# Optimization experiments

Measured on AMD Instinct MI355X. Metric: run time of the kernel, lower is better.

Reference implementation:

```python
import jax, jax.numpy as jnp
import numpy as np
import math

D_MODEL = 1024
N_HEADS = 16
D_K = D_MODEL // N_HEADS
THRESH = 0.1  # attention probs below this are zeroed


def setup_inputs() -> dict:
    key = jax.random.key(0)
    ks = jax.random.split(key, 9)
    B, S, D = 2, 2048, D_MODEL
    scale = 1.0 / math.sqrt(D)
    x = jax.random.normal(ks[0], (B, S, D), dtype=jnp.float32)
    Wq = jax.random.normal(ks[1], (D, D), dtype=jnp.float32) * scale
    bq = jax.random.normal(ks[2], (D,), dtype=jnp.float32) * 0.01
    Wk = jax.random.normal(ks[3], (D, D), dtype=jnp.float32) * scale
    bk = jax.random.normal(ks[4], (D,), dtype=jnp.float32) * 0.01
    Wv = jax.random.normal(ks[5], (D, D), dtype=jnp.float32) * scale
    bv = jax.random.normal(ks[6], (D,), dtype=jnp.float32) * 0.01
    Wo = jax.random.normal(ks[7], (D, D), dtype=jnp.float32) * scale
    bo = jax.random.normal(ks[8], (D,), dtype=jnp.float32) * 0.01
    return {"x": x, "Wq": Wq, "bq": bq, "Wk": Wk, "bk": bk,
            "Wv": Wv, "bv": bv, "Wo": Wo, "bo": bo}


def _split_heads(t):
    B, S, D = t.shape
    return t.reshape(B, S, N_HEADS, D_K).transpose(0, 2, 1, 3)  # [B,H,S,dk]


def reference(x, Wq, bq, Wk, bk, Wv, bv, Wo, bo):
    # torch nn.Linear: y = x @ W.T + b
    q = _split_heads(x @ Wq.T + bq)
    k = _split_heads(x @ Wk.T + bk)
    v = _split_heads(x @ Wv.T + bv)
    scores = jnp.einsum('bhqd,bhkd->bhqk', q, k) / math.sqrt(D_K)
    probs = jax.nn.softmax(scores, axis=-1)          # full unmasked softmax (returned)
    keep = probs >= THRESH                            # ~low_attention_mask
    probs_model = jnp.where(keep, probs, 0.0)        # masked_fill; dropout is identity in eval
    ctx = jnp.einsum('bhqk,bhkd->bhqd', probs_model, v)
    B, H, S, dk = ctx.shape
    merged = ctx.transpose(0, 2, 1, 3).reshape(B, S, H * dk)
    out = merged @ Wo.T + bo
    attention_sum = probs.sum(axis=1)                # [B,S,S] sum over heads
    attention_mask = keep.astype(jnp.float32).sum(axis=1)  # [B,S,S]
    return (out, attention_sum, attention_mask)
```

## Files before the change

### kernel.cpp

```cpp
#include <hip/hip_runtime.h>

#define SDIM 2048
#define DDIM 1024
#define NH 16
#define DK 64
#define NB 2
#define MROWS (NB * SDIM)
#define MAXEV 65536
#define EXPC 0.18033688011112f
#define L01 -3.3219281f

typedef _Float16 f16x8 __attribute__((ext_vector_type(8)));
typedef _Float16 f16x4 __attribute__((ext_vector_type(4)));
typedef float f32x4 __attribute__((ext_vector_type(4)));

__device__ __forceinline__ void ld_lds16(const _Float16* g, _Float16* l) {
  __builtin_amdgcn_global_load_lds(
      (const __attribute__((address_space(1))) void*)g,
      (__attribute__((address_space(3))) void*)l, 16, 0, 0);
}

__global__ __launch_bounds__(256) void cvt_f16(
    const float* __restrict__ x, const float* __restrict__ wq,
    const float* __restrict__ wk, const float* __restrict__ wv,
    _Float16* __restrict__ xh, _Float16* __restrict__ wqh,
    _Float16* __restrict__ wkh, _Float16* __restrict__ wvh) {
  int i = blockIdx.x * 256 + threadIdx.x;
  const float* src;
  _Float16* dst;
  int off;
  if (i < 1048576) {
    src = x; dst = xh; off = i;
  } else if (i < 1310720) {
    src = wq; dst = wqh; off = i - 1048576;
  } else if (i < 1572864) {
    src = wk; dst = wkh; off = i - 1310720;
  } else {
    src = wv; dst = wvh; off = i - 1572864;
  }
  float4 v = ((const float4*)src)[off];
  f16x4 h;
  h[0] = (_Float16)v.x; h[1] = (_Float16)v.y;
  h[2] = (_Float16)v.z; h[3] = (_Float16)v.w;
  ((f16x4*)dst)[off] = h;
}

__global__ __launch_bounds__(256, 2) void proj_gemm(
    const _Float16* __restrict__ xh, const _Float16* __restrict__ Wqh,
    const _Float16* __restrict__ Wkh, const _Float16* __restrict__ Wvh,
    const float* __restrict__ bq, const float* __restrict__ bk,
    const float* __restrict__ bv, _Float16* __restrict__ Qo,
    _Float16* __restrict__ Ko, float* __restrict__ Vo) {
  __shared__ _Float16 sA[128 * 64];
  __shared__ _Float16 sB[128 * 64];
  const int t = threadIdx.x;
  const int lane = t & 63, wv = t >> 6;
  const int lr = lane & 15, quad = lane >> 4;
  const int wm = wv >> 1, wn = wv & 1;
  const int m0 = blockIdx.y * 128, n0 = blockIdx.x * 128;
  const int z = blockIdx.z;
  const _Float16* Bp = z == 0 ? Wqh : (z == 1 ? Wkh : Wvh);
  const float* bias = z == 0 ? bq : (z == 1 ? bk : bv);

  const int strow = t >> 3;
  const int stchunk = t & 7;
  const int stsrc = (stchunk ^ (strow & 7)) * 8;

  f32x4 acc[4][4];
#pragma unroll
  for (int i = 0; i < 4; ++i)
#pragma unroll
    for (int j = 0; j < 4; ++j) acc[i][j] = (f32x4){0.f, 0.f, 0.f, 0.f};

  for (int k0 = 0; k0 < DDIM; k0 += 64) {
    __syncthreads();
#pragma unroll
    for (int i = 0; i < 4; ++i) {
      const int row = i * 32 + strow;
      ld_lds16(&xh[(size_t)(m0 + row) * DDIM + k0 + stsrc],
               &sA[row * 64 + stchunk * 8]);
      ld_lds16(&Bp[(size_t)(n0 + row) * DDIM + k0 + stsrc],
               &sB[row * 64 + stchunk * 8]);
    }
    __syncthreads();
    f16x8 af[4][2], bf[4][2];
#pragma unroll
    for (int i = 0; i < 4; ++i)
#pragma unroll
      for (int kk = 0; kk < 2; ++kk) {
        const int ph = ((kk * 4 + quad) ^ (lr & 7)) * 8;
        af[i][kk] = *(const f16x8*)&sA[(wm * 64 + i * 16 + lr) * 64 + ph];
        bf[i][kk] = *(const f16x8*)&sB[(wn * 64 + i * 16 + lr) * 64 + ph];
      }
#pragma unroll
    for (int kk = 0; kk < 2; ++kk)
#pragma unroll
      for (int i = 0; i < 4; ++i)
#pragma unroll
        for (int j = 0; j < 4; ++j)
          acc[i][j] = __builtin_amdgcn_mfma_f32_16x16x32_f16(
              af[i][kk], bf[j][kk], acc[i][j], 0, 0, 0);
  }
#pragma unroll
  for (int j = 0; j < 4; ++j) {
    const int ng = n0 + wn * 64 + j * 16 + lr;
    const float bvv = bias[ng];
    const int h = ng >> 6, d = ng & 63;
#pragma unroll
    for (int i = 0; i < 4; ++i) {
#pragma unroll
      for (int r = 0; r < 4; ++r) {
        const int mg = m0 + wm * 64 + i * 16 + quad * 4 + r;
        const int b = mg >> 11, s = mg & 2047;
        const float o = acc[i][j][r] + bvv;
        const size_t off = ((size_t)(b * NH + h) * SDIM + s) * DK + d;
        if (z == 0)
          Qo[off] = (_Float16)(o * EXPC);
        else if (z == 1)
          Ko[off] = (_Float16)o;
        else
          Vo[off] = o;
      }
    }
  }
}

__global__ __launch_bounds__(256, 6) void attn_denom(
    const _Float16* __restrict__ Q, const _Float16* __restrict__ K,
    float* __restrict__ laOut) {
  __shared__ __align__(16) _Float16 KS[3 * 4096];
  const int t = threadIdx.x;
  const int lane = t & 63, wave = t >> 6;
  const int quad = lane >> 4, lr = lane & 15;
  const int id = blockIdx.x;
  const int xcd = id & 7, inner = id >> 3;
  const int bh = xcd * 4 + (inner >> 5);
  const int q0 = (inner & 31) * 64;
  const _Float16* Qh = Q + (size_t)bh * SDIM * DK;
  const _Float16* Kh = K + (size_t)bh * SDIM * DK;
  const size_t qoff = (size_t)(q0 + wave * 16 + lr) * DK + quad * 8;
  const f16x8 aq0 = *(const f16x8*)&Qh[qoff];
  const f16x8 aq1 = *(const f16x8*)&Qh[qoff + 32];
  const int strow = t >> 3, stchunk = t & 7;
  const int stsrc = (stchunk ^ (strow & 7)) * 8;
  const int ph0 = (quad ^ (lr & 7)) * 8;
  const int ph1 = ((4 + quad) ^ (lr & 7)) * 8;

#define STAGE_DN(KT, BUF)                                                  \
  {                                                                        \
    _Pragma("unroll") for (int i = 0; i < 2; ++i)                          \
        ld_lds16(&Kh[(size_t)((KT)*64 + i * 32 + strow) * DK + stsrc],     \
                 &(BUF)[(i * 32 + strow) * 64 + stchunk * 8]);             \
  }

#define COMPUTE_DN(BUF)                                                   \
  _Pragma("unroll") for (int c = 0; c < 4; ++c) {                         \
    f16x8 b0 = *(const f16x8*)&(BUF)[(c * 16 + lr) * 64 + ph0];           \
    f16x8 b1 = *(const f16x8*)&(BUF)[(c * 16 + lr) * 64 + ph1];           \
    f32x4 acc = {0.f, 0.f, 0.f, 0.f};                                     \
    acc = __builtin_amdgcn_mfma_f32_16x16x32_f16(aq0, b0, acc, 0, 0, 0);  \
    acc = __builtin_amdgcn_mfma_f32_16x16x32_f16(aq1, b1, acc, 0, 0, 0);  \
    _Pragma("unroll") for (int r = 0; r < 4; ++r)                         \
        dsum[r] += __builtin_amdgcn_exp2f(acc[r]);                        \
  }

  float dsum[4] = {0.f, 0.f, 0.f, 0.f};
  STAGE_DN(0, KS);
  int cb = 0;
#pragma unroll 1
  for (int kt = 0; kt < 32; ++kt) {
    const int nb_ = cb == 2 ? 0 : cb + 1;
    if (kt + 1 < 32) STAGE_DN(kt + 1, KS + nb_ * 4096);
    asm volatile("" ::: "memory");
    if (kt + 1 < 32)
      asm volatile("s_waitcnt vmcnt(2)" ::: "memory");
    else
      asm volatile("s_waitcnt vmcnt(0)" ::: "memory");
    __builtin_amdgcn_s_barrier();
    asm volatile("" ::: "memory");
    COMPUTE_DN(KS + cb * 4096);
    cb = nb_;
  }
#pragma unroll
  for (int m = 1; m < 16; m <<= 1)
#pragma unroll
    for (int r = 0; r < 4; ++r)
      dsum[r] += __shfl_xor(dsum[r], m, 64);
  if (lr == 0) {
#pragma unroll
    for (int r = 0; r < 4; ++r)
      laOut[(size_t)bh * SDIM + q0 + wave * 16 + quad * 4 + r] =
          -__builtin_amdgcn_logf(dsum[r]);
  }
#undef STAGE_DN
#undef COMPUTE_DN
}

__global__ __launch_bounds__(256, 6) void attn_pass2(
    const _Float16* __restrict__ Q, const _Float16* __restrict__ K,
    const float* __restrict__ la, float* __restrict__ attSum,
    float* __restrict__ attMask, float4* __restrict__ ev,
    int* __restrict__ ecnt) {
  __shared__ __align__(16) _Float16 KS[3 * 4096];
  float* Tbuf = (float*)KS;
  const int t = threadIdx.x;
  const int lane = t & 63, wave = t >> 6;
  const int quad = lane >> 4, lr = lane & 15;
  const int id = blockIdx.x;
  const int xcd = id & 7, inner = id >> 3;
  const int b = xcd >> 2;
  const int q0 = (((xcd >> 1) & 1) * 16 + (inner >> 4)) * 64;
  const int k0 = ((xcd & 1) * 16 + (inner & 15)) * 64;
  const int strow = t >> 3, stchunk = t & 7;
  const int stsrc = (stchunk ^ (strow & 7)) * 8;
  const int ph0 = (quad ^ (lr & 7)) * 8;
  const int ph1 = ((4 + quad) ^ (lr & 7)) * 8;

  const size_t qbase = ((size_t)(b * NH) * SDIM + q0 + wave * 16 + lr) * DK;
  const size_t dbase = (size_t)(b * NH) * SDIM + q0 + wave * 16 + quad * 4;
  const size_t hstep = (size_t)SDIM * DK;

  float asum[4][4] = {};
  float mxr[4] = {-1e30f, -1e30f, -1e30f, -1e30f};

  f16x8 a0c, a1c, a0n, a1n;
  float4 lavc, lavn;

#define STAGE_H(H, BUF)                                                      \
  {                                                                          \
    const _Float16* Kp =                                                     \
        K + (size_t)(b * NH + (H)) * hstep + (size_t)k0 * DK;                \
    _Pragma("unroll") for (int i = 0; i < 2; ++i)                            \
        ld_lds16(&Kp[(size_t)(i * 32 + strow) * DK + stsrc],                 \
                 &(BUF)[(i * 32 + strow) * 64 + stchunk * 8]);               \
  }

#define LOADQ_H(H, A0, A1, LV)                                               \
  {                                                                          \
    const size_t ho = (size_t)(H)*hstep;                                     \
    A0 = *(const f16x8*)&Q[qbase + ho + quad * 8];                           \
    A1 = *(const f16x8*)&Q[qbase + ho + 32 + quad * 8];                      \
    LV = *(const float4*)&la[dbase + (size_t)(H)*SDIM];                      \
  }

#define COMPUTE_H(BUF, A0, A1, LV)                                           \
  {                                                                          \
    const float lar[4] = {LV.x, LV.y, LV.z, LV.w};                           \
    _Pragma("unroll") for (int c = 0; c < 4; ++c) {                          \
      f16x8 b0 = *(const f16x8*)&(BUF)[(c * 16 + lr) * 64 + ph0];            \
      f16x8 b1 = *(const f16x8*)&(BUF)[(c * 16 + lr) * 64 + ph1];            \
      f32x4 acc = {0.f, 0.f, 0.f, 0.f};                                      \
      acc = __builtin_amdgcn_mfma_f32_16x16x32_f16(A0, b0, acc, 0, 0, 0);    \
      acc = __builtin_amdgcn_mfma_f32_16x16x32_f16(A1, b1, acc, 0, 0, 0);    \
      _Pragma("unroll") for (int r = 0; r < 4; ++r) {                        \
        const float arg = acc[r] + lar[r];                                   \
        mxr[r] = fmaxf(mxr[r], arg);                                         \
        asum[c][r] += __builtin_amdgcn_exp2f(arg);                           \
      }                                                                      \
    }                                                                        \
  }

  STAGE_H(0, KS);
  LOADQ_H(0, a0c, a1c, lavc);
  int cb = 0;
#pragma unroll 1
  for (int h = 0; h < NH; ++h) {
    const int nb_ = cb == 2 ? 0 : cb + 1;
    if (h + 1 < NH) {
      STAGE_H(h + 1, KS + nb_ * 4096);
      LOADQ_H(h + 1, a0n, a1n, lavn);
    }
    asm volatile("" ::: "memory");
    if (h + 1 < NH)
      asm volatile("s_waitcnt vmcnt(5)" ::: "memory");
    else
      asm volatile("s_waitcnt vmcnt(0)" ::: "memory");
    __builtin_amdgcn_s_barrier();
    asm volatile("" ::: "memory");
    COMPUTE_H(KS + cb * 4096, a0c, a1c, lavc);
    if (h + 1 < NH) {
      a0c = a0n; a1c = a1n; lavc = lavn;
    }
    cb = nb_;
  }
#undef STAGE_H
#undef LOADQ_H
#undef COMPUTE_H

  const float mx =
      fmaxf(fmaxf(mxr[0], mxr[1]), fmaxf(mxr[2], mxr[3]));
  if (__any(mx >= L01)) {
    float amask[4][4] = {};
#pragma unroll 1
    for (int h = 0; h < NH; ++h) {
      const _Float16* Kp =
          K + (size_t)(b * NH + h) * hstep + (size_t)k0 * DK;
      const size_t ho = (size_t)h * hstep;
      const f16x8 aq0 = *(const f16x8*)&Q[qbase + ho + quad * 8];
      const f16x8 aq1 = *(const f16x8*)&Q[qbase + ho + 32 + quad * 8];
      const float4 l4 = *(const float4*)&la[dbase + (size_t)h * SDIM];
      const float lar[4] = {l4.x, l4.y, l4.z, l4.w};
#pragma unroll 1
      for (int c = 0; c < 4; ++c) {
        const f16x8 b0 = *(const f16x8*)&Kp[(c * 16 + lr) * DK + quad * 8];
        const f16x8 b1 = *(const f16x8*)&Kp[(c * 16 + lr) * DK + 32 + quad * 8];
        f32x4 acc = {0.f, 0.f, 0.f, 0.f};
        acc = __builtin_amdgcn_mfma_f32_16x16x32_f16(aq0, b0, acc, 0, 0, 0);
        acc = __builtin_amdgcn_mfma_f32_16x16x32_f16(aq1, b1, acc, 0, 0, 0);
#pragma unroll 1
        for (int r = 0; r < 4; ++r) {
          const float p = __builtin_amdgcn_exp2f(acc[r] + lar[r]);
          if (p >= 0.1f) {
            amask[c][r] += 1.0f;
            int idx = atomicAdd(ecnt, 1);
            if (idx < MAXEV)
              ev[idx] = make_float4(
                  __int_as_float(b * NH + h),
                  __int_as_float(q0 + wave * 16 + quad * 4 + r),
                  __int_as_float(k0 + c * 16 + lr), p);
          }
        }
      }
    }
#pragma unroll
    for (int c = 0; c < 4; ++c)
#pragma unroll
      for (int r = 0; r < 4; ++r)
        if (amask[c][r] != 0.0f) {
          const size_t row = (size_t)(b * SDIM) + q0 + wave * 16 + quad * 4 + r;
          attMask[row * SDIM + k0 + c * 16 + lr] = amask[c][r];
        }
  }
  const int g8 = t >> 3;
  const int l8 = (t & 7) * 4;
  __syncthreads();
#pragma unroll
  for (int c = 0; c < 4; ++c)
#pragma unroll
    for (int r = 0; r < 4; ++r)
      Tbuf[(wave * 16 + quad * 4 + r) * 68 + c * 16 + lr] = asum[c][r];
  __syncthreads();
#pragma unroll
  for (int p = 0; p < 2; ++p)
#pragma unroll
    for (int qh = 0; qh < 2; ++qh) {
      const int row = p * 32 + g8, col = qh * 32 + l8;
      f32x4 v = *(const f32x4*)&Tbuf[row * 68 + col];
      __builtin_nontemporal_store(
          v, (f32x4*)&attSum[((size_t)(b * SDIM) + q0 + row) * SDIM + k0 + col]);
    }
}

__global__ __launch_bounds__(64) void apply_events(
    const float4* __restrict__ ev, const int* __restrict__ ecnt,
    const float* __restrict__ V, float* __restrict__ merged,
    int* __restrict__ flags) {
  int n = *ecnt;
  if (n > MAXEV) n = MAXEV;
  const int d = threadIdx.x;
  for (int e = blockIdx.x; e < n; e += gridDim.x) {
    float4 r = ev[e];
    int bh = __float_as_int(r.x);
    int q = __float_as_int(r.y);
    int kc = __float_as_int(r.z);
    float p = r.w;
    int b = bh >> 4, h = bh & 15;
    atomicAdd(&merged[((size_t)(b * SDIM + q)) * DDIM + h * DK + d],
              p * V[((size_t)bh * SDIM + kc) * DK + d]);
    if (d == 0) flags[b * SDIM + q] = 1;
  }
}

__global__ __launch_bounds__(256) void out_gemm(const float* __restrict__ A,
                                                const float* __restrict__ W,
                                                const float* __restrict__ bias,
                                                float* __restrict__ out,
                                                const int* __restrict__ flags) {
  __shared__ float As[16][68];
  __shared__ float Ws[16][68];
  __shared__ int anyF;
  const int t = threadIdx.x;
  const int tx = t & 15, ty = t >> 4;
  const int m0 = blockIdx.y * 64;
  const int n0 = blockIdx.x * 64;
  if (t == 0) anyF = 0;
  __syncthreads();
  if (t < 64 && flags[m0 + t]) anyF = 1;
  __syncthreads();
  const int nb = n0 + tx * 4;
  const float4 bv = *(const float4*)&bias[nb];
  if (!anyF) {
#pragma unroll
    for (int r = 0; r < 4; ++r)
      *(float4*)&out[(size_t)(m0 + ty * 4 + r) * DDIM + nb] = bv;
    return;
  }
  const int lr = t >> 2;
  const int lc = (t & 3) * 4;
  float acc[4][4] = {};
  for (int k0 = 0; k0 < DDIM; k0 += 16) {
    __syncthreads();
    float4 av = *(const float4*)&A[(size_t)(m0 + lr) * DDIM + k0 + lc];
    float4 wv = *(const float4*)&W[(size_t)(n0 + lr) * DDIM + k0 + lc];
    As[lc + 0][lr] = av.x; As[lc + 1][lr] = av.y;
    As[lc + 2][lr] = av.z; As[lc + 3][lr] = av.w;
    Ws[lc + 0][lr] = wv.x; Ws[lc + 1][lr] = wv.y;
    Ws[lc + 2][lr] = wv.z; Ws[lc + 3][lr] = wv.w;
    __syncthreads();
#pragma unroll
    for (int kk = 0; kk < 16; ++kk) {
      float4 a4 = *(const float4*)&As[kk][ty * 4];
      float4 b4 = *(const float4*)&Ws[kk][tx * 4];
      const float a[4] = {a4.x, a4.y, a4.z, a4.w};
      const float b[4] = {b4.x, b4.y, b4.z, b4.w};
#pragma unroll
      for (int r = 0; r < 4; ++r)
#pragma unroll
        for (int c = 0; c < 4; ++c)
          acc[r][c] = fmaf(a[r], b[c], acc[r][c]);
    }
  }
#pragma unroll
  for (int r = 0; r < 4; ++r) {
    float4 o;
    o.x = acc[r][0] + bv.x;
    o.y = acc[r][1] + bv.y;
    o.z = acc[r][2] + bv.z;
    o.w = acc[r][3] + bv.w;
    *(float4*)&out[(size_t)(m0 + ty * 4 + r) * DDIM + nb] = o;
  }
}

extern "C" void kernel_launch(void* const* d_in, const int* in_sizes, int n_in,
                              void* d_out, int out_size, void* d_ws,
                              size_t ws_size, hipStream_t stream) {
  const float* x = (const float*)d_in[0];
  const float* Wq = (const float*)d_in[1];
  const float* bq = (const float*)d_in[2];
  const float* Wk = (const float*)d_in[3];
  const float* bk = (const float*)d_in[4];
  const float* Wv = (const float*)d_in[5];
  const float* bv = (const float*)d_in[6];
  const float* Wo = (const float*)d_in[7];
  const float* bo = (const float*)d_in[8];

  float* out = (float*)d_out;
  float* attSum = out + (size_t)MROWS * DDIM;
  float* attMask = attSum + (size_t)NB * SDIM * SDIM;

  char* ws = (char*)d_ws;
  const size_t bigF = (size_t)MROWS * DDIM * sizeof(float);
  const size_t bigH = (size_t)MROWS * DDIM * sizeof(_Float16);
  const size_t wH = (size_t)DDIM * DDIM * sizeof(_Float16);
  _Float16* Qh = (_Float16*)ws;  ws += bigH;
  _Float16* Kh = (_Float16*)ws;  ws += bigH;
  float* V = (float*)ws;         ws += bigF;
  float* merged = (float*)ws;    ws += bigF;
  _Float16* xh = (_Float16*)ws;  ws += bigH;
  _Float16* Wqh = (_Float16*)ws; ws += wH;
  _Float16* Wkh = (_Float16*)ws; ws += wH;
  _Float16* Wvh = (_Float16*)ws; ws += wH;
  float* laBuf = (float*)ws;     ws += (size_t)NB * NH * SDIM * sizeof(float);
  float4* ev = (float4*)ws;      ws += (size_t)MAXEV * sizeof(float4);
  int* flags = (int*)ws;         ws += (size_t)MROWS * sizeof(int);
  int* ecnt = (int*)ws;          ws += 16;

  hipMemsetAsync(merged, 0, bigF, stream);
  hipMemsetAsync(flags, 0, (size_t)MROWS * sizeof(int), stream);
  hipMemsetAsync(ecnt, 0, 16, stream);
  hipMemsetAsync(attMask, 0, (size_t)NB * SDIM * SDIM * sizeof(float), stream);

  dim3 blk(256);
  cvt_f16<<<dim3(7168), blk, 0, stream>>>(x, Wq, Wk, Wv, xh, Wqh, Wkh, Wvh);
  proj_gemm<<<dim3(8, 32, 3), blk, 0, stream>>>(xh, Wqh, Wkh, Wvh, bq, bk, bv,
                                                Qh, Kh, V);
  attn_denom<<<dim3(1024), blk, 0, stream>>>(Qh, Kh, laBuf);
  attn_pass2<<<dim3(2048), blk, 0, stream>>>(Qh, Kh, laBuf, attSum,
                                             attMask, ev, ecnt);
  apply_events<<<dim3(256), dim3(64), 0, stream>>>(ev, ecnt, V, merged, flags);
  out_gemm<<<dim3(16, 64), blk, 0, stream>>>(merged, Wo, bo, out, flags);
}
```

Before: 254.2 us.

## Double-buffer projection GEMM and deepen K prefetch in attention kernels

The projection GEMM moves from a single LDS buffer with two syncthreads per k-step to a double-buffered pipeline. It prefetches the next tile with global_load_lds while computing the current one, under explicit vmcnt waits. The two attention passes go from three to four LDS buffers and prefetch two tiles ahead; occupancy drops from 6 to 4 blocks per CU to make room. In pass2 the log-denominator is folded into the MFMA accumulator init, the max reduction is narrowed, and MFMA sections are wrapped in s_setprio. The aim is to hide global load latency behind compute, at the cost of lower occupancy and hand-tuned waitcnt counts that must match the load order exactly.

```diff
diff --git a/kernel.cpp b/kernel.cpp
--- a/kernel.cpp
+++ b/kernel.cpp
@@ -51,8 +51,8 @@
     const float* __restrict__ bq, const float* __restrict__ bk,
     const float* __restrict__ bv, _Float16* __restrict__ Qo,
     _Float16* __restrict__ Ko, float* __restrict__ Vo) {
-  __shared__ _Float16 sA[128 * 64];
-  __shared__ _Float16 sB[128 * 64];
+  __shared__ _Float16 sA[2][128 * 64];
+  __shared__ _Float16 sB[2][128 * 64];
   const int t = threadIdx.x;
   const int lane = t & 63, wv = t >> 6;
   const int lr = lane & 15, quad = lane >> 4;
@@ -72,26 +72,39 @@
 #pragma unroll
     for (int j = 0; j < 4; ++j) acc[i][j] = (f32x4){0.f, 0.f, 0.f, 0.f};
 
+#define PSTAGE(K0, IB)                                                     \
+  {                                                                        \
+    _Pragma("unroll") for (int i = 0; i < 4; ++i) {                        \
+      const int row = i * 32 + strow;                                      \
+      ld_lds16(&xh[(size_t)(m0 + row) * DDIM + (K0) + stsrc],              \
+               &sA[IB][row * 64 + stchunk * 8]);                           \
+      ld_lds16(&Bp[(size_t)(n0 + row) * DDIM + (K0) + stsrc],              \
+               &sB[IB][row * 64 + stchunk * 8]);                           \
+    }                                                                      \
+  }
+
+  PSTAGE(0, 0);
+  int cur = 0;
+#pragma unroll 1
   for (int k0 = 0; k0 < DDIM; k0 += 64) {
-    __syncthreads();
-#pragma unroll
-    for (int i = 0; i < 4; ++i) {
-      const int row = i * 32 + strow;
-      ld_lds16(&xh[(size_t)(m0 + row) * DDIM + k0 + stsrc],
-               &sA[row * 64 + stchunk * 8]);
-      ld_lds16(&Bp[(size_t)(n0 + row) * DDIM + k0 + stsrc],
-               &sB[row * 64 + stchunk * 8]);
-    }
-    __syncthreads();
+    if (k0 + 64 < DDIM) PSTAGE(k0 + 64, cur ^ 1);
+    asm volatile("" ::: "memory");
+    if (k0 + 64 < DDIM)
+      asm volatile("s_waitcnt vmcnt(8)" ::: "memory");
+    else
+      asm volatile("s_waitcnt vmcnt(0)" ::: "memory");
+    __builtin_amdgcn_s_barrier();
+    asm volatile("" ::: "memory");
     f16x8 af[4][2], bf[4][2];
 #pragma unroll
     for (int i = 0; i < 4; ++i)
 #pragma unroll
       for (int kk = 0; kk < 2; ++kk) {
         const int ph = ((kk * 4 + quad) ^ (lr & 7)) * 8;
-        af[i][kk] = *(const f16x8*)&sA[(wm * 64 + i * 16 + lr) * 64 + ph];
-        bf[i][kk] = *(const f16x8*)&sB[(wn * 64 + i * 16 + lr) * 64 + ph];
+        af[i][kk] = *(const f16x8*)&sA[cur][(wm * 64 + i * 16 + lr) * 64 + ph];
+        bf[i][kk] = *(const f16x8*)&sB[cur][(wn * 64 + i * 16 + lr) * 64 + ph];
       }
+    __builtin_amdgcn_s_setprio(1);
 #pragma unroll
     for (int kk = 0; kk < 2; ++kk)
 #pragma unroll
@@ -100,7 +113,12 @@
         for (int j = 0; j < 4; ++j)
           acc[i][j] = __builtin_amdgcn_mfma_f32_16x16x32_f16(
               af[i][kk], bf[j][kk], acc[i][j], 0, 0, 0);
-  }
+    __builtin_amdgcn_s_setprio(0);
+    asm volatile("" ::: "memory");
+    __builtin_amdgcn_s_barrier();
+    cur ^= 1;
+  }
+#undef PSTAGE
 #pragma unroll
   for (int j = 0; j < 4; ++j) {
     const int ng = n0 + wn * 64 + j * 16 + lr;
@@ -125,10 +143,10 @@
   }
 }
 
-__global__ __launch_bounds__(256, 6) void attn_denom(
+__global__ __launch_bounds__(256, 4) void attn_denom(
     const _Float16* __restrict__ Q, const _Float16* __restrict__ K,
     float* __restrict__ laOut) {
-  __shared__ __align__(16) _Float16 KS[3 * 4096];
+  __shared__ __align__(16) _Float16 KS[4 * 4096];
   const int t = threadIdx.x;
   const int lane = t & 63, wave = t >> 6;
   const int quad = lane >> 4, lr = lane & 15;
@@ -146,10 +164,10 @@
   const int ph0 = (quad ^ (lr & 7)) * 8;
   const int ph1 = ((4 + quad) ^ (lr & 7)) * 8;
 
-#define STAGE_DN(KT, BUF)                                                  \
+#define STAGE_DN(KP, BUF)                                                  \
   {                                                                        \
     _Pragma("unroll") for (int i = 0; i < 2; ++i)                          \
-        ld_lds16(&Kh[(size_t)((KT)*64 + i * 32 + strow) * DK + stsrc],     \
+        ld_lds16(&(KP)[(size_t)(i * 32 + strow) * DK + stsrc],             \
                  &(BUF)[(i * 32 + strow) * 64 + stchunk * 8]);             \
   }
 
@@ -165,21 +183,31 @@
   }
 
   float dsum[4] = {0.f, 0.f, 0.f, 0.f};
-  STAGE_DN(0, KS);
+  const _Float16* kp = Kh;
+  STAGE_DN(kp, KS);
+  kp += 64 * DK;
+  STAGE_DN(kp, KS + 4096);
+  kp += 64 * DK;
   int cb = 0;
 #pragma unroll 1
   for (int kt = 0; kt < 32; ++kt) {
-    const int nb_ = cb == 2 ? 0 : cb + 1;
-    if (kt + 1 < 32) STAGE_DN(kt + 1, KS + nb_ * 4096);
-    asm volatile("" ::: "memory");
-    if (kt + 1 < 32)
+    if (kt + 2 < 32) {
+      STAGE_DN(kp, KS + ((cb + 2) & 3) * 4096);
+      kp += 64 * DK;
+    }
+    asm volatile("" ::: "memory");
+    if (kt + 2 < 32)
+      asm volatile("s_waitcnt vmcnt(4)" ::: "memory");
+    else if (kt + 1 < 32)
       asm volatile("s_waitcnt vmcnt(2)" ::: "memory");
     else
       asm volatile("s_waitcnt vmcnt(0)" ::: "memory");
     __builtin_amdgcn_s_barrier();
     asm volatile("" ::: "memory");
+    __builtin_amdgcn_s_setprio(1);
     COMPUTE_DN(KS + cb * 4096);
-    cb = nb_;
+    __builtin_amdgcn_s_setprio(0);
+    cb = (cb + 1) & 3;
   }
 #pragma unroll
   for (int m = 1; m < 16; m <<= 1)
@@ -196,12 +224,12 @@
 #undef COMPUTE_DN
 }
 
-__global__ __launch_bounds__(256, 6) void attn_pass2(
+__global__ __launch_bounds__(256, 4) void attn_pass2(
     const _Float16* __restrict__ Q, const _Float16* __restrict__ K,
     const float* __restrict__ la, float* __restrict__ attSum,
     float* __restrict__ attMask, float4* __restrict__ ev,
     int* __restrict__ ecnt) {
-  __shared__ __align__(16) _Float16 KS[3 * 4096];
+  __shared__ __align__(16) _Float16 KS[4 * 4096];
   float* Tbuf = (float*)KS;
   const int t = threadIdx.x;
   const int lane = t & 63, wave = t >> 6;
@@ -221,74 +249,83 @@
   const size_t hstep = (size_t)SDIM * DK;
 
   float asum[4][4] = {};
-  float mxr[4] = {-1e30f, -1e30f, -1e30f, -1e30f};
+  float mx01 = -1e30f, mx23 = -1e30f;
 
   f16x8 a0c, a1c, a0n, a1n;
   float4 lavc, lavn;
 
-#define STAGE_H(H, BUF)                                                      \
+#define STAGE1(KP, BUF)                                                      \
   {                                                                          \
-    const _Float16* Kp =                                                     \
-        K + (size_t)(b * NH + (H)) * hstep + (size_t)k0 * DK;                \
     _Pragma("unroll") for (int i = 0; i < 2; ++i)                            \
-        ld_lds16(&Kp[(size_t)(i * 32 + strow) * DK + stsrc],                 \
+        ld_lds16(&(KP)[(size_t)(i * 32 + strow) * DK + stsrc],               \
                  &(BUF)[(i * 32 + strow) * 64 + stchunk * 8]);               \
   }
 
-#define LOADQ_H(H, A0, A1, LV)                                               \
+#define LOADQ1(QP, LAP, A0, A1, LV)                                          \
   {                                                                          \
-    const size_t ho = (size_t)(H)*hstep;                                     \
-    A0 = *(const f16x8*)&Q[qbase + ho + quad * 8];                           \
-    A1 = *(const f16x8*)&Q[qbase + ho + 32 + quad * 8];                      \
-    LV = *(const float4*)&la[dbase + (size_t)(H)*SDIM];                      \
-  }
-
-#define COMPUTE_H(BUF, A0, A1, LV)                                           \
+    A0 = *(const f16x8*)&(QP)[quad * 8];                                     \
+    A1 = *(const f16x8*)&(QP)[32 + quad * 8];                                \
+    LV = *(const float4*)(LAP);                                              \
+  }
+
+#define COMPUTE1(BUF, A0, A1, LV)                                            \
   {                                                                          \
-    const float lar[4] = {LV.x, LV.y, LV.z, LV.w};                           \
+    const f32x4 cinit = {LV.x, LV.y, LV.z, LV.w};                            \
     _Pragma("unroll") for (int c = 0; c < 4; ++c) {                          \
       f16x8 b0 = *(const f16x8*)&(BUF)[(c * 16 + lr) * 64 + ph0];            \
       f16x8 b1 = *(const f16x8*)&(BUF)[(c * 16 + lr) * 64 + ph1];            \
-      f32x4 acc = {0.f, 0.f, 0.f, 0.f};                                      \
+      f32x4 acc = cinit;                  \
       acc = __builtin_amdgcn_mfma_f32_16x16x32_f16(A0, b0, acc, 0, 0, 0);    \
       acc = __builtin_amdgcn_mfma_f32_16x16x32_f16(A1, b1, acc, 0, 0, 0);    \
-      _Pragma("unroll") for (int r = 0; r < 4; ++r) {                        \
-        const float arg = acc[r] + lar[r];                                   \
-        mxr[r] = fmaxf(mxr[r], arg);                                         \
-        asum[c][r] += __builtin_amdgcn_exp2f(arg);                           \
-      }                                                                      \
+      mx01 = fmaxf(fmaxf(acc[0], acc[1]), mx01);                 \
+      mx23 = fmaxf(fmaxf(acc[2], acc[3]), mx23);                             \
+      asum[c][0] += __builtin_amdgcn_exp2f(acc[0]);                          \
+      asum[c][1] += __builtin_amdgcn_exp2f(acc[1]);                          \
+      asum[c][2] += __builtin_amdgcn_exp2f(acc[2]);                          \
+      asum[c][3] += __builtin_amdgcn_exp2f(acc[3]);                          \
     }                                                                        \
   }
 
-  STAGE_H(0, KS);
-  LOADQ_H(0, a0c, a1c, lavc);
+  const _Float16* kp = K + (size_t)(b * NH) * hstep + (size_t)k0 * DK;
+  const _Float16* qp = Q + qbase;
+  const float* lap = la + dbase;
+  STAGE1(kp, KS);
+  kp += hstep;
+  STAGE1(kp, KS + 4096);
+  kp += hstep;
+  LOADQ1(qp, lap, a0c, a1c, lavc);
+  qp += hstep; lap += SDIM;
   int cb = 0;
 #pragma unroll 1
   for (int h = 0; h < NH; ++h) {
-    const int nb_ = cb == 2 ? 0 : cb + 1;
+    if (h + 2 < NH) {
+      STAGE1(kp, KS + ((cb + 2) & 3) * 4096);
+      kp += hstep;
+    }
     if (h + 1 < NH) {
-      STAGE_H(h + 1, KS + nb_ * 4096);
-      LOADQ_H(h + 1, a0n, a1n, lavn);
-    }
-    asm volatile("" ::: "memory");
-    if (h + 1 < NH)
-      asm volatile("s_waitcnt vmcnt(5)" ::: "memory");
+      LOADQ1(qp, lap, a0n, a1n, lavn);
+      qp += hstep; lap += SDIM;
+    }
+    asm volatile("" ::: "memory");
+    if (h == NH - 1)
+      asm volatile("s_waitcnt vmcnt(6)" ::: "memory");
     else
-      asm volatile("s_waitcnt vmcnt(0)" ::: "memory");
+      asm volatile("s_waitcnt vmcnt(10)" ::: "memory");
     __builtin_amdgcn_s_barrier();
     asm volatile("" ::: "memory");
-    COMPUTE_H(KS + cb * 4096, a0c, a1c, lavc);
+    __builtin_amdgcn_s_setprio(1);
+    COMPUTE1(KS + cb * 4096, a0c, a1c, lavc);
+    __builtin_amdgcn_s_setprio(0);
     if (h + 1 < NH) {
       a0c = a0n; a1c = a1n; lavc = lavn;
     }
-    cb = nb_;
-  }
-#undef STAGE_H
-#undef LOADQ_H
-#undef COMPUTE_H
-
-  const float mx =
-      fmaxf(fmaxf(mxr[0], mxr[1]), fmaxf(mxr[2], mxr[3]));
+    cb = (cb + 1) & 3;
+  }
+#undef STAGE1
+#undef LOADQ1
+#undef COMPUTE1
+
+  const float mx = fmaxf(mx01, mx23);
   if (__any(mx >= L01)) {
     float amask[4][4] = {};
 #pragma unroll 1
```

Result: no change. 250.2 us (-1.6%).
